# Optimization experiments

Measured on AMD Instinct MI355X. Metric: run time of the kernel, lower is better.

The kernel has to match this reference:

```python
import jax, jax.numpy as jnp
import numpy as np

N, D0, D1, HID, OUT = 4096, 256, 128, 64, 16
R, M, K, PROJ = 3, 2, 2, 128  # meta-path rels, same-type rels, schema rels, attn hidden


def setup_inputs() -> dict:
    key = jax.random.key(0)
    ks = jax.random.split(key, 24)
    g = lambda i, shape, s: jax.random.normal(ks[i], shape, jnp.float32) * s
    return {
        "features0": g(0, (N, D0), 1.0),
        "features1": g(1, (N, D1), 1.0),
        # row-scale adjacencies so aggregated features stay O(1)
        "adj_same": jax.random.uniform(ks[2], (M, N, N), jnp.float32) / N,
        "adj_meta": jax.random.uniform(ks[3], (R, N, N), jnp.float32) / N,
        "adj_schema": jax.random.uniform(ks[4], (K, N, N), jnp.float32) / N,
        "Wm0": g(5, (D0, HID), D0 ** -0.5), "bm0": jnp.zeros((HID,), jnp.float32),
        "Wm1": g(6, (D1, HID), D1 ** -0.5), "bm1": jnp.zeros((HID,), jnp.float32),
        "Wa": g(7, (HID, PROJ), HID ** -0.5), "ba": jnp.zeros((PROJ,), jnp.float32),
        "qa": g(8, (PROJ,), PROJ ** -0.5),
        "ws": g(9, (HID, 1), HID ** -0.5),
        "Wc1": g(10, (HID, PROJ), HID ** -0.5), "bc1": jnp.zeros((PROJ,), jnp.float32),
        "wc2": g(11, (PROJ, 1), PROJ ** -0.5),
        "Wt1": g(12, (HID, PROJ), HID ** -0.5), "bt1": jnp.zeros((PROJ,), jnp.float32),
        "wt2": g(13, (PROJ, 1), PROJ ** -0.5),
        "Wp": g(14, (HID, OUT), HID ** -0.5), "bp": jnp.zeros((OUT,), jnp.float32),
    }


def reference(features0, features1, adj_same, adj_meta, adj_schema,
              Wm0, bm0, Wm1, bm1, Wa, ba, qa, ws, Wc1, bc1, wc2,
              Wt1, bt1, wt2, Wp, bp):
    # per-type feature mapping: tanh(Linear(x))
    h0 = jnp.tanh(features0 @ Wm0 + bm0)  # [N, HID]
    h1 = jnp.tanh(features1 @ Wm1 + bm1)  # [N, HID]

    # --- Dif_Classes_AGG: meta-path aggregation + semantic attention over R relations ---
    hr = jnp.tanh(jnp.einsum('rij,jd->rid', adj_meta, h0))        # [R, N, HID]
    s = jnp.mean(jnp.tanh(hr @ Wa + ba) @ qa, axis=1)             # [R]
    beta_r = jax.nn.softmax(s)                                    # [R]
    relation_agg = jnp.einsum('r,rnd->nd', beta_r, hr)            # [N, HID]

    # --- Weight_Schema: schema-matrix aggregation with per-node softmax over K ---
    zk = jnp.einsum('kij,jd->kid', adj_schema, h1)                # [K, N, HID]
    beta_k = jax.nn.softmax(jnp.squeeze(zk @ ws, -1), axis=0)     # [K, N]
    item_classes_agg = jnp.einsum('kn,knd->nd', beta_k, zk)       # [N, HID]

    # --- Classes_Relation_AGG: same-type (item-item) aggregation over M relations ---
    ym = jnp.tanh(jnp.einsum('mij,jd->mid', adj_same, item_classes_agg))  # [M, N, HID]
    wm = jnp.squeeze(jnp.tanh(ym @ Wc1 + bc1) @ wc2, -1)          # [M, N]
    beta_m = jax.nn.softmax(wm, axis=0)                           # [M, N]
    item_item = jnp.einsum('mn,mnd->nd', beta_m, ym)              # [N, HID]

    # --- AggAttention over the two module outputs ---
    Hs = jnp.stack([relation_agg, item_item], axis=1)             # [N, 2, HID]
    wt = jnp.squeeze(jnp.tanh(Hs @ Wt1 + bt1) @ wt2, -1)          # [N, 2]
    beta_t = jax.nn.softmax(wt, axis=1)[..., None]                # [N, 2, 1]
    H = jnp.sum(beta_t * Hs, axis=1)                              # [N, HID]

    return (H @ Wp + bp, H)
```

## Files before the change

### kernel.cpp

```cpp
#include <hip/hip_runtime.h>

#define NODES 4096

typedef float f32x4 __attribute__((ext_vector_type(4)));
typedef float f32x8 __attribute__((ext_vector_type(8)));
typedef __bf16 bf16x8 __attribute__((ext_vector_type(8)));
typedef unsigned short u16x8 __attribute__((ext_vector_type(8)));

__device__ __forceinline__ unsigned short f2bf(float x) {
    unsigned u = __builtin_bit_cast(unsigned, x);
    return (unsigned short)((u + 0x7fffu + ((u >> 16) & 1u)) >> 16);
}

__device__ __forceinline__ void glds16(const void* g, void* l) {
    __builtin_amdgcn_global_load_lds(
        (const __attribute__((address_space(1))) unsigned int*)g,
        (__attribute__((address_space(3))) unsigned int*)l,
        16, 0, 0);
}

__global__ __launch_bounds__(256) void prep_h(
    const float* __restrict__ f0, const float* __restrict__ f1,
    const float* __restrict__ Wm0, const float* __restrict__ bm0,
    const float* __restrict__ Wm1, const float* __restrict__ bm1,
    unsigned short* __restrict__ hT0, unsigned short* __restrict__ hT1)
{
    const int d = threadIdx.x & 63;
    int n = blockIdx.x * 4 + (threadIdx.x >> 6);
    n = __builtin_amdgcn_readfirstlane(n);
    const float* r0 = f0 + (size_t)n * 256;
    float a0 = bm0[d];
#pragma unroll 8
    for (int k = 0; k < 256; ++k) a0 = fmaf(r0[k], Wm0[k * 64 + d], a0);
    hT0[(size_t)d * NODES + n] = f2bf(tanhf(a0));
    const float* r1 = f1 + (size_t)n * 128;
    float a1 = bm1[d];
#pragma unroll 8
    for (int k = 0; k < 128; ++k) a1 = fmaf(r1[k], Wm1[k * 64 + d], a1);
    hT1[(size_t)d * NODES + n] = f2bf(tanhf(a1));
}

__global__ __launch_bounds__(256) void adj_gemm(
    const float* __restrict__ A0, const float* __restrict__ A1,
    const float* __restrict__ A2, const float* __restrict__ A3,
    const float* __restrict__ A4,
    const unsigned short* __restrict__ hTa, const unsigned short* __restrict__ hTb,
    int split, float* __restrict__ outBase, unsigned tanhMask,
    int khBits, int klen)
{
    __shared__ __align__(16) char smem[2 * 49152];

    const int job = blockIdx.y;
    const float* adj = job == 0 ? A0 : job == 1 ? A1 : job == 2 ? A2 : job == 3 ? A3 : A4;
    const unsigned short* hT = (job < split) ? hTa : hTb;
    const bool doTanh = (tanhMask >> job) & 1u;

    const int bx = blockIdx.x;
    const int group = bx >> khBits;
    const int kh = bx & ((1 << khBits) - 1);
    const int kc0 = kh * klen;
    const int nc = klen >> 7;
    const int n0 = group * 64;

    const int lane = threadIdx.x & 63;
    const int wid = threadIdx.x >> 6;
    const int fr = lane & 15, fg = lane >> 4;

    const char* aBase = (const char*)adj;
    const char* hBase = (const char*)hT;
    const char* aSrc[8]; int aDst[8];
#pragma unroll
    for (int i = 0; i < 8; ++i) {
        const int seg = wid * 8 + i;
        const int rowc = seg * 2 + (lane >> 5);
        const int kbs = (lane & 31) * 16;
        const int kb = kbs ^ ((rowc & 7) << 4);
        aSrc[i] = aBase + (size_t)(n0 + rowc) * (NODES * 4) + (size_t)kc0 * 4 + kb;
        aDst[i] = seg * 1024;
    }
    const char* bSrc[4]; int bDst[4];
#pragma unroll
    for (int i = 0; i < 4; ++i) {
        const int seg = wid * 4 + i;
        const int d = seg * 4 + (lane >> 4);
        const int kbs = (lane & 15) * 16;
        const int kb = kbs ^ ((d & 7) << 4);
        bSrc[i] = hBase + (size_t)d * (NODES * 2) + (size_t)kc0 * 2 + kb;
        bDst[i] = 32768 + seg * 1024;
    }

#define STAGE(c)                                                          \
    {                                                                     \
        char* dstb = smem + ((c) & 1) * 49152;                            \
        const size_t aoff = (size_t)(c) * 512;                            \
        const size_t boff = (size_t)(c) * 256;                            \
        _Pragma("unroll")                                                 \
        for (int i = 0; i < 8; ++i) glds16(aSrc[i] + aoff, dstb + aDst[i]); \
        _Pragma("unroll")                                                 \
        for (int i = 0; i < 4; ++i) glds16(bSrc[i] + boff, dstb + bDst[i]); \
    }

    f32x4 acc0 = {0.f,0.f,0.f,0.f}, acc1 = {0.f,0.f,0.f,0.f};
    f32x4 acc2 = {0.f,0.f,0.f,0.f}, acc3 = {0.f,0.f,0.f,0.f};

    const int rowA = wid * 16 + fr;
    const int swzA = (rowA & 7) << 4;

    STAGE(0);
    STAGE(1);

    for (int c = 0; c < nc; ++c) {
        if (c + 1 < nc) { asm volatile("s_waitcnt vmcnt(12)" ::: "memory"); }
        else            { asm volatile("s_waitcnt vmcnt(0)"  ::: "memory"); }
        __builtin_amdgcn_sched_barrier(0);
        __builtin_amdgcn_s_barrier();
        __builtin_amdgcn_sched_barrier(0);

        const char* bb = smem + (c & 1) * 49152;
        const char* aRow = bb + rowA * 512;
#pragma unroll
        for (int ks = 0; ks < 4; ++ks) {
            const int kb = ks * 128 + fg * 32;
            f32x4 alo = *(const f32x4*)(aRow + ((kb)      ^ swzA));
            f32x4 ahi = *(const f32x4*)(aRow + ((kb + 16) ^ swzA));
            f32x8 av = __builtin_shufflevector(alo, ahi, 0,1,2,3,4,5,6,7);
            bf16x8 af = __builtin_convertvector(av, bf16x8);
            const int kb2 = ks * 64 + fg * 16;
            {
                const int dcol = 0 * 16 + fr;
                u16x8 bv = *(const u16x8*)(bb + 32768 + dcol * 256 + (kb2 ^ ((dcol & 7) << 4)));
                acc0 = __builtin_amdgcn_mfma_f32_16x16x32_bf16(af, __builtin_bit_cast(bf16x8, bv), acc0, 0, 0, 0);
            }
            {
                const int dcol = 1 * 16 + fr;
                u16x8 bv = *(const u16x8*)(bb + 32768 + dcol * 256 + (kb2 ^ ((dcol & 7) << 4)));
                acc1 = __builtin_amdgcn_mfma_f32_16x16x32_bf16(af, __builtin_bit_cast(bf16x8, bv), acc1, 0, 0, 0);
            }
            {
                const int dcol = 2 * 16 + fr;
                u16x8 bv = *(const u16x8*)(bb + 32768 + dcol * 256 + (kb2 ^ ((dcol & 7) << 4)));
                acc2 = __builtin_amdgcn_mfma_f32_16x16x32_bf16(af, __builtin_bit_cast(bf16x8, bv), acc2, 0, 0, 0);
            }
            {
                const int dcol = 3 * 16 + fr;
                u16x8 bv = *(const u16x8*)(bb + 32768 + dcol * 256 + (kb2 ^ ((dcol & 7) << 4)));
                acc3 = __builtin_amdgcn_mfma_f32_16x16x32_bf16(af, __builtin_bit_cast(bf16x8, bv), acc3, 0, 0, 0);
            }
        }

        __builtin_amdgcn_sched_barrier(0);
        __builtin_amdgcn_s_barrier();
        __builtin_amdgcn_sched_barrier(0);
        if (c + 2 < nc) STAGE(c + 2);
    }
#undef STAGE

    float* outC = outBase + (size_t)((job << khBits) | kh) * (NODES * 64);
    float* Cw = outC + (size_t)(n0 + wid * 16 + fg * 4) * 64 + fr;
#pragma unroll
    for (int j = 0; j < 4; ++j) {
        float v0 = acc0[j], v1 = acc1[j], v2 = acc2[j], v3 = acc3[j];
        if (doTanh) { v0 = tanhf(v0); v1 = tanhf(v1); v2 = tanhf(v2); v3 = tanhf(v3); }
        Cw[(size_t)j * 64 + 0]  = v0; Cw[(size_t)j * 64 + 16] = v1;
        Cw[(size_t)j * 64 + 32] = v2; Cw[(size_t)j * 64 + 48] = v3;
    }
}

__global__ __launch_bounds__(128) void stage_c(
    const float* __restrict__ agg, const float* __restrict__ Wa,
    const float* __restrict__ ba, const float* __restrict__ qa,
    const float* __restrict__ wsv, float* __restrict__ sacc,
    unsigned short* __restrict__ iccT)
{
    const int n = blockIdx.x;
    const int p = threadIdx.x;
    __shared__ float rs[3][2];
    __shared__ float ru[2][2];

    const float* h0p = agg + (size_t)n * 64;
    const float* h1p = agg + ((size_t)NODES + n) * 64;
    const float* h2p = agg + ((size_t)2 * NODES + n) * 64;
    float a0 = ba[p], a1 = a0, a2 = a0;
#pragma unroll 8
    for (int d = 0; d < 64; ++d) {
        float w = Wa[d * 128 + p];
        a0 = fmaf(h0p[d], w, a0);
        a1 = fmaf(h1p[d], w, a1);
        a2 = fmaf(h2p[d], w, a2);
    }
    float qv = qa[p];
    float v0 = tanhf(a0) * qv, v1 = tanhf(a1) * qv, v2 = tanhf(a2) * qv;

    const float* z0 = agg + ((size_t)3 * NODES + n) * 64;
    const float* z1 = agg + ((size_t)4 * NODES + n) * 64;
    float u0 = (p < 64) ? z0[p] * wsv[p] : 0.f;
    float u1 = (p < 64) ? z1[p] * wsv[p] : 0.f;

#pragma unroll
    for (int off = 32; off; off >>= 1) {
        v0 += __shfl_down(v0, off); v1 += __shfl_down(v1, off); v2 += __shfl_down(v2, off);
        u0 += __shfl_down(u0, off); u1 += __shfl_down(u1, off);
    }
    if ((p & 63) == 0) {
        int w = p >> 6;
        rs[0][w] = v0; rs[1][w] = v1; rs[2][w] = v2;
        ru[0][w] = u0; ru[1][w] = u1;
    }
    __syncthreads();
    if (p < 3) atomicAdd(&sacc[p], rs[p][0] + rs[p][1]);

    float U0 = ru[0][0] + ru[0][1];
    float U1 = ru[1][0] + ru[1][1];
    float mx = fmaxf(U0, U1);
    float e0 = expf(U0 - mx), e1 = expf(U1 - mx);
    float inv = 1.f / (e0 + e1);
    if (p < 64) {
        float icc = (e0 * z0[p] + e1 * z1[p]) * inv;
        iccT[(size_t)p * NODES + n] = f2bf(icc);
    }
}

__global__ __launch_bounds__(256) void finalize(
    const float* __restrict__ agg, const float* __restrict__ ymp,
    const float* __restrict__ sacc,
    const float* __restrict__ Wc1, const float* __restrict__ bc1, const float* __restrict__ wc2,
    const float* __restrict__ Wt1, const float* __restrict__ bt1, const float* __restrict__ wt2,
    const float* __restrict__ Wp, const float* __restrict__ bp,
    float* __restrict__ out)
{
    __shared__ float sWc[64 * 128];
    __shared__ float sWp[64 * 16];
    __shared__ float sY0[2][64], sY1[2][64];
    __shared__ float sHs0[2][64], sHs1[2][64], sHv[2][64];
    __shared__ float rA[2][2], rB[2][2];

    const int t = threadIdx.x;
    for (int i = t; i < 64 * 128; i += 256) sWc[i] = Wc1[i];
    for (int i = t; i < 64 * 16; i += 256) sWp[i] = Wp[i];

    float s0 = sacc[0] * (1.f / NODES), s1 = sacc[1] * (1.f / NODES), s2 = sacc[2] * (1.f / NODES);
    float sm = fmaxf(s0, fmaxf(s1, s2));
    float b0 = expf(s0 - sm), b1 = expf(s1 - sm), b2 = expf(s2 - sm);
    float bi = 1.f / (b0 + b1 + b2);
    b0 *= bi; b1 *= bi; b2 *= bi;

    const int sub = t >> 7;
    const int p = t & 127;
    const int wiH = p >> 6;
    const float bcv = bc1[p], wcv = wc2[p], btv = bt1[p], wtv = wt2[p];
    __syncthreads();

    for (int it = 0; it < 8; ++it) {
        const int n = blockIdx.x * 16 + it * 2 + sub;
        if (p < 64) {
            const size_t NN64 = (size_t)NODES * 64;
            float ya = ymp[(size_t)n * 64 + p]            + ymp[NN64 + (size_t)n * 64 + p];
            float yb = ymp[2 * NN64 + (size_t)n * 64 + p] + ymp[3 * NN64 + (size_t)n * 64 + p];
            sY0[sub][p] = tanhf(ya);
            sY1[sub][p] = tanhf(yb);
            sHs0[sub][p] = b0 * agg[(size_t)n * 64 + p]
                         + b1 * agg[((size_t)NODES + n) * 64 + p]
                         + b2 * agg[((size_t)2 * NODES + n) * 64 + p];
        }
        __syncthreads();
        float ac0 = bcv, ac1 = bcv;
#pragma unroll 8
        for (int d = 0; d < 64; ++d) {
            float w = sWc[d * 128 + p];
            ac0 = fmaf(sY0[sub][d], w, ac0);
            ac1 = fmaf(sY1[sub][d], w, ac1);
        }
        float v0 = tanhf(ac0) * wcv, v1 = tanhf(ac1) * wcv;
#pragma unroll
        for (int off = 32; off; off >>= 1) { v0 += __shfl_down(v0, off); v1 += __shfl_down(v1, off); }
        if ((p & 63) == 0) { rA[sub][wiH] = v0; rB[sub][wiH] = v1; }
        __syncthreads();
        float wm0 = rA[sub][0] + rA[sub][1];
        float wm1 = rB[sub][0] + rB[sub][1];
        float mm = fmaxf(wm0, wm1);
        float g0 = expf(wm0 - mm), g1 = expf(wm1 - mm);
        float gi = 1.f / (g0 + g1);
        g0 *= gi; g1 *= gi;
        if (p < 64) sHs1[sub][p] = g0 * sY0[sub][p] + g1 * sY1[sub][p];
        __syncthreads();

        float at0 = btv, at1 = btv;
#pragma unroll 8
        for (int d = 0; d < 64; ++d) {
            float w = Wt1[d * 128 + p];
            at0 = fmaf(sHs0[sub][d], w, at0);
            at1 = fmaf(sHs1[sub][d], w, at1);
        }
        float q0 = tanhf(at0) * wtv, q1 = tanhf(at1) * wtv;
#pragma unroll
        for (int off = 32; off; off >>= 1) { q0 += __shfl_down(q0, off); q1 += __shfl_down(q1, off); }
        if ((p & 63) == 0) { rA[sub][wiH] = q0; rB[sub][wiH] = q1; }
        __syncthreads();
        float t0 = rA[sub][0] + rA[sub][1];
        float t1 = rB[sub][0] + rB[sub][1];
        float tm = fmaxf(t0, t1);
        float c0 = expf(t0 - tm), c1 = expf(t1 - tm);
        float ci = 1.f / (c0 + c1);
        c0 *= ci; c1 *= ci;
        if (p < 64) {
            float H = c0 * sHs0[sub][p] + c1 * sHs1[sub][p];
            sHv[sub][p] = H;
            out[(size_t)NODES * 16 + (size_t)n * 64 + p] = H;
        }
        __syncthreads();
        if (p < 16) {
            float a = bp[p];
#pragma unroll 8
            for (int d = 0; d < 64; ++d) a = fmaf(sHv[sub][d], sWp[d * 16 + p], a);
            out[(size_t)n * 16 + p] = a;
        }
        __syncthreads();
    }
}

extern "C" void kernel_launch(void* const* d_in, const int* in_sizes, int n_in,
                              void* d_out, int out_size, void* d_ws, size_t ws_size,
                              hipStream_t stream)
{
    const float* f0   = (const float*)d_in[0];
    const float* f1   = (const float*)d_in[1];
    const float* adjS = (const float*)d_in[2];
    const float* adjM = (const float*)d_in[3];
    const float* adjK = (const float*)d_in[4];
    const float* Wm0  = (const float*)d_in[5];
    const float* bm0  = (const float*)d_in[6];
    const float* Wm1  = (const float*)d_in[7];
    const float* bm1  = (const float*)d_in[8];
    const float* Wa   = (const float*)d_in[9];
    const float* ba   = (const float*)d_in[10];
    const float* qa   = (const float*)d_in[11];
    const float* wsv  = (const float*)d_in[12];
    const float* Wc1  = (const float*)d_in[13];
    const float* bc1  = (const float*)d_in[14];
    const float* wc2  = (const float*)d_in[15];
    const float* Wt1  = (const float*)d_in[16];
    const float* bt1  = (const float*)d_in[17];
    const float* wt2  = (const float*)d_in[18];
    const float* Wp   = (const float*)d_in[19];
    const float* bpv  = (const float*)d_in[20];
    float* out = (float*)d_out;

    char* ws = (char*)d_ws;
    unsigned short* hT0  = (unsigned short*)(ws);
    unsigned short* hT1  = (unsigned short*)(ws + 524288);
    unsigned short* iccT = (unsigned short*)(ws + 1048576);
    float* agg           = (float*)(ws + 1572864);
    float* ymp           = (float*)(ws + 4718592);
    float* sacc          = (float*)(ws + 8912896);

    hipMemsetAsync(sacc, 0, 64, stream);
    prep_h<<<dim3(1024), dim3(256), 0, stream>>>(f0, f1, Wm0, bm0, Wm1, bm1, hT0, hT1);

    const size_t NNs = (size_t)NODES * NODES;
    adj_gemm<<<dim3(64, 5), dim3(256), 0, stream>>>(
        adjM, adjM + NNs, adjM + 2 * NNs, adjK, adjK + NNs,
        hT0, hT1, 3, agg, 0x7u, 0, 4096);
    stage_c<<<dim3(4096), dim3(128), 0, stream>>>(agg, Wa, ba, qa, wsv, sacc, iccT);
    adj_gemm<<<dim3(128, 2), dim3(256), 0, stream>>>(
        adjS, adjS + NNs, adjS, adjS, adjS,
        iccT, iccT, 5, ymp, 0x0u, 1, 2048);
    finalize<<<dim3(256), dim3(256), 0, stream>>>(
        agg, ymp, sacc, Wc1, bc1, wc2, Wt1, bt1, wt2, Wp, bpv, out);
}
```

Measured before the change: 256.1 us.

## Use triple-buffered 64-wide K chunks in adj_gemm for more loads in flight

Halves the K chunk per stage from 128 to 64 and moves from double to triple buffering of LDS (72KB instead of 96KB), with launch bounds requesting two blocks per CU. The aim is to keep more global-to-LDS loads in flight and fit two blocks per CU, hiding HBM latency on this memory-bound adjacency streaming GEMM. The cost is twice as many barriers and waitcnt points per K range, and the tightened register budget may cause spills.

```diff
diff --git a/kernel.cpp b/kernel.cpp
--- a/kernel.cpp
+++ b/kernel.cpp
@@ -40,7 +40,7 @@
     hT1[(size_t)d * NODES + n] = f2bf(tanhf(a1));
 }
 
-__global__ __launch_bounds__(256) void adj_gemm(
+__global__ __launch_bounds__(256, 2) void adj_gemm(
     const float* __restrict__ A0, const float* __restrict__ A1,
     const float* __restrict__ A2, const float* __restrict__ A3,
     const float* __restrict__ A4,
@@ -48,7 +48,7 @@
     int split, float* __restrict__ outBase, unsigned tanhMask,
     int khBits, int klen)
 {
-    __shared__ __align__(16) char smem[2 * 49152];
+    __shared__ __align__(16) char smem[3 * 24576];
 
     const int job = blockIdx.y;
     const float* adj = job == 0 ? A0 : job == 1 ? A1 : job == 2 ? A2 : job == 3 ? A3 : A4;
@@ -59,67 +59,66 @@
     const int group = bx >> khBits;
     const int kh = bx & ((1 << khBits) - 1);
     const int kc0 = kh * klen;
-    const int nc = klen >> 7;
+    const int nc = klen >> 6;
     const int n0 = group * 64;
 
     const int lane = threadIdx.x & 63;
     const int wid = threadIdx.x >> 6;
     const int fr = lane & 15, fg = lane >> 4;
 
-    const char* aBase = (const char*)adj;
-    const char* hBase = (const char*)hT;
-    const char* aSrc[8]; int aDst[8];
-#pragma unroll
-    for (int i = 0; i < 8; ++i) {
-        const int seg = wid * 8 + i;
-        const int rowc = seg * 2 + (lane >> 5);
-        const int kbs = (lane & 31) * 16;
-        const int kb = kbs ^ ((rowc & 7) << 4);
-        aSrc[i] = aBase + (size_t)(n0 + rowc) * (NODES * 4) + (size_t)kc0 * 4 + kb;
-        aDst[i] = seg * 1024;
-    }
-    const char* bSrc[4]; int bDst[4];
+    const char* aSrc[4]; int aDst[4];
 #pragma unroll
     for (int i = 0; i < 4; ++i) {
         const int seg = wid * 4 + i;
-        const int d = seg * 4 + (lane >> 4);
-        const int kbs = (lane & 15) * 16;
-        const int kb = kbs ^ ((d & 7) << 4);
-        bSrc[i] = hBase + (size_t)d * (NODES * 2) + (size_t)kc0 * 2 + kb;
-        bDst[i] = 32768 + seg * 1024;
-    }
-
-#define STAGE(c)                                                          \
-    {                                                                     \
-        char* dstb = smem + ((c) & 1) * 49152;                            \
-        const size_t aoff = (size_t)(c) * 512;                            \
-        const size_t boff = (size_t)(c) * 256;                            \
-        _Pragma("unroll")                                                 \
-        for (int i = 0; i < 8; ++i) glds16(aSrc[i] + aoff, dstb + aDst[i]); \
-        _Pragma("unroll")                                                 \
-        for (int i = 0; i < 4; ++i) glds16(bSrc[i] + boff, dstb + bDst[i]); \
+        const int r = seg * 4 + (lane >> 4);
+        const int sb = ((lane & 15) * 16) ^ ((r & 7) << 4);
+        aSrc[i] = (const char*)adj + (size_t)(n0 + r) * (NODES * 4) + (size_t)kc0 * 4 + sb;
+        aDst[i] = seg * 1024;
+    }
+    const char* bSrc[2]; int bDst[2];
+#pragma unroll
+    for (int i = 0; i < 2; ++i) {
+        const int seg = wid * 2 + i;
+        const int d = seg * 8 + (lane >> 3);
+        const int sb = ((lane & 7) * 16) ^ ((d & 7) << 4);
+        bSrc[i] = (const char*)hT + (size_t)d * (NODES * 2) + (size_t)kc0 * 2 + sb;
+        bDst[i] = 16384 + seg * 1024;
+    }
+
+#define STAGE(c, dstb)                                                        \
+    {                                                                         \
+        const size_t aoff = (size_t)(c) * 256;                                \
+        const size_t boff = (size_t)(c) * 128;                                \
+        _Pragma("unroll")                                                     \
+        for (int i = 0; i < 4; ++i) glds16(aSrc[i] + aoff, (dstb) + aDst[i]); \
+        _Pragma("unroll")                                                     \
+        for (int i = 0; i < 2; ++i) glds16(bSrc[i] + boff, (dstb) + bDst[i]); \
     }
 
     f32x4 acc0 = {0.f,0.f,0.f,0.f}, acc1 = {0.f,0.f,0.f,0.f};
     f32x4 acc2 = {0.f,0.f,0.f,0.f}, acc3 = {0.f,0.f,0.f,0.f};
 
     const int rowA = wid * 16 + fr;
-    const int swzA = (rowA & 7) << 4;
-
-    STAGE(0);
-    STAGE(1);
-
+    const int swzA = (fr & 7) << 4;
+
+    STAGE(0, smem);
+    STAGE(1, smem + 24576);
+    STAGE(2, smem + 2 * 24576);
+
+    int cur = 0;
     for (int c = 0; c < nc; ++c) {
-        if (c + 1 < nc) { asm volatile("s_waitcnt vmcnt(12)" ::: "memory"); }
-        else            { asm volatile("s_waitcnt vmcnt(0)"  ::: "memory"); }
+        const int rem = nc - c;
+        if (rem >= 3)      { asm volatile("s_waitcnt vmcnt(12)" ::: "memory"); }
+        else if (rem == 2) { asm volatile("s_waitcnt vmcnt(6)"  ::: "memory"); }
+        else               { asm volatile("s_waitcnt vmcnt(0)"  ::: "memory"); }
         __builtin_amdgcn_sched_barrier(0);
         __builtin_amdgcn_s_barrier();
         __builtin_amdgcn_sched_barrier(0);
 
-        const char* bb = smem + (c & 1) * 49152;
-        const char* aRow = bb + rowA * 512;
-#pragma unroll
-        for (int ks = 0; ks < 4; ++ks) {
+        char* bb = smem + cur * 24576;
+        const char* aRow = bb + rowA * 256;
+#pragma unroll
+        for (int ks = 0; ks < 2; ++ks) {
             const int kb = ks * 128 + fg * 32;
             f32x4 alo = *(const f32x4*)(aRow + ((kb)      ^ swzA));
             f32x4 ahi = *(const f32x4*)(aRow + ((kb + 16) ^ swzA));
@@ -128,22 +127,22 @@
             const int kb2 = ks * 64 + fg * 16;
             {
                 const int dcol = 0 * 16 + fr;
-                u16x8 bv = *(const u16x8*)(bb + 32768 + dcol * 256 + (kb2 ^ ((dcol & 7) << 4)));
+                u16x8 bv = *(const u16x8*)(bb + 16384 + dcol * 128 + (kb2 ^ ((dcol & 7) << 4)));
                 acc0 = __builtin_amdgcn_mfma_f32_16x16x32_bf16(af, __builtin_bit_cast(bf16x8, bv), acc0, 0, 0, 0);
             }
             {
                 const int dcol = 1 * 16 + fr;
-                u16x8 bv = *(const u16x8*)(bb + 32768 + dcol * 256 + (kb2 ^ ((dcol & 7) << 4)));
+                u16x8 bv = *(const u16x8*)(bb + 16384 + dcol * 128 + (kb2 ^ ((dcol & 7) << 4)));
                 acc1 = __builtin_amdgcn_mfma_f32_16x16x32_bf16(af, __builtin_bit_cast(bf16x8, bv), acc1, 0, 0, 0);
             }
             {
                 const int dcol = 2 * 16 + fr;
-                u16x8 bv = *(const u16x8*)(bb + 32768 + dcol * 256 + (kb2 ^ ((dcol & 7) << 4)));
+                u16x8 bv = *(const u16x8*)(bb + 16384 + dcol * 128 + (kb2 ^ ((dcol & 7) << 4)));
                 acc2 = __builtin_amdgcn_mfma_f32_16x16x32_bf16(af, __builtin_bit_cast(bf16x8, bv), acc2, 0, 0, 0);
             }
             {
                 const int dcol = 3 * 16 + fr;
-                u16x8 bv = *(const u16x8*)(bb + 32768 + dcol * 256 + (kb2 ^ ((dcol & 7) << 4)));
+                u16x8 bv = *(const u16x8*)(bb + 16384 + dcol * 128 + (kb2 ^ ((dcol & 7) << 4)));
                 acc3 = __builtin_amdgcn_mfma_f32_16x16x32_bf16(af, __builtin_bit_cast(bf16x8, bv), acc3, 0, 0, 0);
             }
         }
@@ -151,7 +150,8 @@
         __builtin_amdgcn_sched_barrier(0);
         __builtin_amdgcn_s_barrier();
         __builtin_amdgcn_sched_barrier(0);
-        if (c + 2 < nc) STAGE(c + 2);
+        if (c + 3 < nc) STAGE(c + 3, bb);
+        cur = (cur == 2) ? 0 : cur + 1;
     }
 #undef STAGE
 
```

Result: no change. 259.0 us (+1.2%).
